# Kernel optimization log

Measured on AMD Instinct MI355X. Metric: run time of the kernel, lower is better.

The kernel has to match this reference:

```python
import math
import jax, jax.numpy as jnp
import numpy as np

B, T, DIN, D, L, K = 32, 4096, 256, 256, 2, 4
EPS = 1e-5
MIN_TS, MAX_TS = 10.0, 2000.0


def setup_inputs() -> dict:
    key = jax.random.key(0)
    ks = jax.random.split(key, 6)
    s = lambda k, shape: jax.random.normal(k, shape, jnp.float32) * 0.05
    return dict(
        x=jax.random.normal(ks[0], (B, T, DIN), jnp.float32),
        enc_w=s(ks[1], (D, DIN)),
        enc_b=jnp.zeros((D,), jnp.float32),
        enc_ln_g=jnp.ones((D,), jnp.float32),
        enc_ln_b=jnp.zeros((D,), jnp.float32),
        in_proj_w=s(ks[2], (L, 2 * D, D)),
        in_proj_b=jnp.zeros((L, 2 * D), jnp.float32),
        conv_w=s(ks[3], (L, D, K)),
        conv_b=jnp.zeros((L, D), jnp.float32),
        out_proj_w=s(ks[4], (L, D, D)),
        out_proj_b=jnp.zeros((L, D), jnp.float32),
        lnf_g=jnp.ones((D,), jnp.float32),
        lnf_b=jnp.zeros((D,), jnp.float32),
    )


def _ln(x, g, b):
    m = x.mean(-1, keepdims=True)
    v = ((x - m) ** 2).mean(-1, keepdims=True)
    return (x - m) * jax.lax.rsqrt(v + EPS) * g + b


def reference(x, enc_w, enc_b, enc_ln_g, enc_ln_b, in_proj_w, in_proj_b,
              conv_w, conv_b, out_proj_w, out_proj_b, lnf_g, lnf_b):
    # multi-timescale decay buffer (fixed, not learned)
    tau = jnp.exp(jnp.linspace(math.log(MIN_TS), math.log(MAX_TS), D))
    decay = jnp.exp(-1.0 / tau).astype(x.dtype)  # [D]

    def step(carry, x_t):
        h_states, bufs = carry  # [L,B,D], [L,B,D,K]
        # encoder: Linear -> LayerNorm -> ReLU
        h = jax.nn.relu(_ln(x_t @ enc_w.T + enc_b, enc_ln_g, enc_ln_b))
        new_h, new_buf = [], []
        for i in range(L):  # small fixed layer count
            xz = h @ in_proj_w[i].T + in_proj_b[i]          # [B,2D]
            x_in, z = xz[:, :D], xz[:, D:]
            # rolling depthwise-conv buffer: shift left, append x_in
            buf = jnp.concatenate([bufs[i][:, :, 1:], x_in[:, :, None]], axis=-1)  # [B,D,K]
            conv_out = jax.nn.silu(jnp.einsum('bdk,dk->bd', buf, conv_w[i]) + conv_b[i])
            hi = decay * h_states[i] + (1.0 - decay) * conv_out  # diagonal SSM update
            out = (hi * jax.nn.silu(z)) @ out_proj_w[i].T + out_proj_b[i]
            h = h + out  # residual
            new_h.append(hi)
            new_buf.append(buf)
        return (jnp.stack(new_h), jnp.stack(new_buf)), _ln(h, lnf_g, lnf_b)

    init = (jnp.zeros((L, B, D), x.dtype), jnp.zeros((L, B, D, K), x.dtype))
    _, ys = jax.lax.scan(step, init, jnp.swapaxes(x, 0, 1))  # ys: [T,B,D]
    return jnp.swapaxes(ys, 0, 1)  # [B,T,D]
```

## Files before the change

kernel.cpp:

```cpp
#include <hip/hip_runtime.h>
#include <hip/hip_bf16.h>
#include <math.h>

#define BB 32
#define TT 4096
#define DD 256
#define LL 2
#define NC 64
#define CH 64
#define MM (BB*TT)
#define EPSV 1e-5f

typedef __bf16 bf16;
typedef __attribute__((ext_vector_type(8))) __bf16 bf16x8;
typedef __attribute__((ext_vector_type(4))) __bf16 bf16x4;
typedef __attribute__((ext_vector_type(2))) __bf16 bf16x2;
typedef __attribute__((ext_vector_type(4))) float f32x4;

__device__ __forceinline__ float decay_of(int d) {
    const float l0 = 2.302585092994046f;
    const float l1 = 7.6009024595420815f;
    float lt = l0 + (float)d * (l1 - l0) * (1.0f / 255.0f);
    return expf(-expf(-lt));
}
__device__ __forceinline__ float silu_f(float v) { return v / (1.0f + expf(-v)); }

__global__ void cvtw_k(const float* __restrict__ we, const float* __restrict__ wi,
                       const float* __restrict__ wo, bf16* __restrict__ de,
                       bf16* __restrict__ di, bf16* __restrict__ dk)
{
    int i = blockIdx.x * 1024 + threadIdx.x;
    if (i < 65536)            de[i] = (bf16)we[i];
    else if (i < 327680)      di[i - 65536] = (bf16)wi[i - 65536];
    else if (i < 458752)      dk[i - 327680] = (bf16)wo[i - 327680];
}

template<int SRCF32, int EPI>
__global__ __launch_bounds__(256, 2)
void gemm_k(const void* __restrict__ Asrc,
            const bf16* __restrict__ W,
            const float* __restrict__ bias,
            const float* __restrict__ g1, const float* __restrict__ b1,
            bf16* __restrict__ O0, bf16* __restrict__ O1,
            float* __restrict__ Of)
{
    constexpr int NT = 16;
    constexpr int KCS = 8;
    constexpr int NSTAGE = 4;
    constexpr int KKS = 2;
    __shared__ bf16x8 ldsW[2048];

    const int tid = threadIdx.x;
    const int colblk = blockIdx.y * 256;
    const bf16* Wblk = W + (size_t)colblk * 256;

    const int wave = tid >> 6, lane = tid & 63;
    const int r = lane & 15, g4 = lane >> 4;
    const int c4 = g4 * 4;
    const size_t row = (size_t)blockIdx.x * 64 + wave * 16 + r;

    bf16x8 af[8];
    if (SRCF32) {
        const float* ap0 = (const float*)Asrc + row * 256;
        #pragma unroll
        for (int kk = 0; kk < 8; ++kk) {
            const float* ap = ap0 + kk * 32 + g4 * 8;
            float4 f0 = *(const float4*)ap;
            float4 f1 = *(const float4*)(ap + 4);
            bf16x8 t;
            t[0]=(bf16)f0.x; t[1]=(bf16)f0.y; t[2]=(bf16)f0.z; t[3]=(bf16)f0.w;
            t[4]=(bf16)f1.x; t[5]=(bf16)f1.y; t[6]=(bf16)f1.z; t[7]=(bf16)f1.w;
            af[kk] = t;
        }
    } else {
        const bf16* ap0 = (const bf16*)Asrc + row * 256;
        #pragma unroll
        for (int kk = 0; kk < 8; ++kk)
            af[kk] = *(const bf16x8*)(ap0 + kk * 32 + g4 * 8);
    }

    f32x4 acc[NT];
    #pragma unroll
    for (int nt = 0; nt < NT; ++nt) {
        float4 bv = *(const float4*)(bias + colblk + nt * 16 + c4);
        acc[nt] = (f32x4){bv.x, bv.y, bv.z, bv.w};
    }

    #pragma unroll
    for (int s = 0; s < NSTAGE; ++s) {
        if (s) __syncthreads();
        const int sBase = s * KCS;
        #pragma unroll
        for (int i = 0; i < 8; ++i) {
            int idx = tid + i * 256;
            int n   = idx >> 3;
            int kc  = idx & 7;
            int kcg = sBase + kc;
            ldsW[kc * 256 + (n ^ (kcg & 15))] =
                *(const bf16x8*)(Wblk + n * 256 + kcg * 8);
        }
        __syncthreads();
        #pragma unroll
        for (int kk = s * KKS; kk < (s + 1) * KKS; ++kk) {
            const int kcg = kk * 4 + g4;
            const int base = (kcg - sBase) * 256;
            const int swz = kcg & 15;
            #pragma unroll
            for (int nt = 0; nt < NT; ++nt) {
                bf16x8 bfr = ldsW[base + ((nt * 16 + r) ^ swz)];
                acc[nt] = __builtin_amdgcn_mfma_f32_16x16x32_bf16(bfr, af[kk], acc[nt], 0, 0, 0);
            }
        }
    }

    if (EPI == 1) {
        float s = 0.f, q = 0.f;
        #pragma unroll
        for (int nt = 0; nt < NT; ++nt)
            #pragma unroll
            for (int i = 0; i < 4; ++i) { float v = acc[nt][i]; s += v; q += v * v; }
        s += __shfl_xor(s, 16); q += __shfl_xor(q, 16);
        s += __shfl_xor(s, 32); q += __shfl_xor(q, 32);
        float mean = s * (1.0f / 256.0f);
        float rstd = rsqrtf(q * (1.0f / 256.0f) - mean * mean + EPSV);
        #pragma unroll
        for (int nt = 0; nt < NT; ++nt) {
            float4 gg = *(const float4*)(g1 + nt * 16 + c4);
            float4 bb = *(const float4*)(b1 + nt * 16 + c4);
            bf16x4 st;
            st[0] = (bf16)fmaxf((acc[nt][0] - mean) * rstd * gg.x + bb.x, 0.f);
            st[1] = (bf16)fmaxf((acc[nt][1] - mean) * rstd * gg.y + bb.y, 0.f);
            st[2] = (bf16)fmaxf((acc[nt][2] - mean) * rstd * gg.z + bb.z, 0.f);
            st[3] = (bf16)fmaxf((acc[nt][3] - mean) * rstd * gg.w + bb.w, 0.f);
            *(bf16x4*)(O0 + row * 256 + nt * 16 + c4) = st;
        }
    } else if (EPI == 2) {
        #pragma unroll
        for (int nt = 0; nt < NT; ++nt) {
            bf16* p = O0 + row * 256 + nt * 16 + c4;
            bf16x4 hv = *(const bf16x4*)p;
            bf16x4 st;
            #pragma unroll
            for (int i = 0; i < 4; ++i) st[i] = (bf16)(acc[nt][i] + (float)hv[i]);
            *(bf16x4*)p = st;
        }
    } else if (EPI == 3) {
        const int dosilu = (colblk >= 256);
        bf16* dst = dosilu ? O1 : O0;
        #pragma unroll
        for (int nt = 0; nt < NT; ++nt) {
            bf16x4 st;
            #pragma unroll
            for (int i = 0; i < 4; ++i) {
                float v = acc[nt][i];
                if (dosilu) v = silu_f(v);
                st[i] = (bf16)v;
            }
            *(bf16x4*)(dst + row * 256 + nt * 16 + c4) = st;
        }
    } else {
        #pragma unroll
        for (int nt = 0; nt < NT; ++nt) {
            bf16x4 hv = *(const bf16x4*)(O0 + row * 256 + nt * 16 + c4);
            #pragma unroll
            for (int i = 0; i < 4; ++i) acc[nt][i] += (float)hv[i];
        }
        float s = 0.f, q = 0.f;
        #pragma unroll
        for (int nt = 0; nt < NT; ++nt)
            #pragma unroll
            for (int i = 0; i < 4; ++i) { float v = acc[nt][i]; s += v; q += v * v; }
        s += __shfl_xor(s, 16); q += __shfl_xor(q, 16);
        s += __shfl_xor(s, 32); q += __shfl_xor(q, 32);
        float mean = s * (1.0f / 256.0f);
        float rstd = rsqrtf(q * (1.0f / 256.0f) - mean * mean + EPSV);
        #pragma unroll
        for (int nt = 0; nt < NT; ++nt) {
            float4 gg = *(const float4*)(g1 + nt * 16 + c4);
            float4 bb = *(const float4*)(b1 + nt * 16 + c4);
            float4 o;
            o.x = (acc[nt][0] - mean) * rstd * gg.x + bb.x;
            o.y = (acc[nt][1] - mean) * rstd * gg.y + bb.y;
            o.z = (acc[nt][2] - mean) * rstd * gg.z + bb.z;
            o.w = (acc[nt][3] - mean) * rstd * gg.w + bb.w;
            *(float4*)(Of + row * 256 + nt * 16 + c4) = o;
        }
    }
}

__global__ void pass1_k(const bf16* __restrict__ xc,
                        const float* __restrict__ cw, const float* __restrict__ cb,
                        float* __restrict__ cfin)
{
    const int d0 = threadIdx.x * 2;
    const int c = blockIdx.x, b = blockIdx.y;
    const int t0 = c * CH;
    const float w00=cw[d0*4+0], w01=cw[d0*4+1], w02=cw[d0*4+2], w03=cw[d0*4+3];
    const float w10=cw[d0*4+4], w11=cw[d0*4+5], w12=cw[d0*4+6], w13=cw[d0*4+7];
    const float bb0 = cb[d0], bb1 = cb[d0+1];
    const float a0 = decay_of(d0), a1 = decay_of(d0+1);
    const size_t base = (size_t)b * TT * 256 + d0;
    float x0m1=0,x0m2=0,x0m3=0, x1m1=0,x1m2=0,x1m3=0;
    if (t0 >= 1) { bf16x2 p = *(const bf16x2*)(xc + base + (size_t)(t0-1)*256); x0m1=(float)p[0]; x1m1=(float)p[1]; }
    if (t0 >= 2) { bf16x2 p = *(const bf16x2*)(xc + base + (size_t)(t0-2)*256); x0m2=(float)p[0]; x1m2=(float)p[1]; }
    if (t0 >= 3) { bf16x2 p = *(const bf16x2*)(xc + base + (size_t)(t0-3)*256); x0m3=(float)p[0]; x1m3=(float)p[1]; }
    float h0 = 0.f, h1 = 0.f;
    for (int t = t0; t < t0 + CH; ++t) {
        bf16x2 p = *(const bf16x2*)(xc + base + (size_t)t * 256);
        float xa = (float)p[0], xb = (float)p[1];
        float v0 = w03*xa + w02*x0m1 + w01*x0m2 + w00*x0m3 + bb0;
        float v1 = w13*xb + w12*x1m1 + w11*x1m2 + w10*x1m3 + bb1;
        h0 = a0*h0 + (1.f-a0)*silu_f(v0);
        h1 = a1*h1 + (1.f-a1)*silu_f(v1);
        x0m3=x0m2; x0m2=x0m1; x0m1=xa;
        x1m3=x1m2; x1m2=x1m1; x1m1=xb;
    }
    *(float2*)(cfin + ((size_t)b*NC + c)*256 + d0) = make_float2(h0, h1);
}

__global__ void scan2_k(const float* __restrict__ cfin, float* __restrict__ cin)
{
    const int d = threadIdx.x, b = blockIdx.x;
    float a = decay_of(d);
    float aC = a;
    #pragma unroll
    for (int j = 0; j < 6; ++j) aC *= aC;
    float H = 0.f;
    for (int c = 0; c < NC; ++c) {
        size_t o = ((size_t)b * NC + c) * 256 + d;
        cin[o] = H;
        H = aC * H + cfin[o];
    }
}

__global__ void pass3_k(const bf16* __restrict__ xc, const float* __restrict__ cin,
                        const float* __restrict__ cw, const float* __restrict__ cb,
                        bf16* __restrict__ szu)
{
    const int d0 = threadIdx.x * 2;
    const int c = blockIdx.x, b = blockIdx.y;
    const int t0 = c * CH;
    const float w00=cw[d0*4+0], w01=cw[d0*4+1], w02=cw[d0*4+2], w03=cw[d0*4+3];
    const float w10=cw[d0*4+4], w11=cw[d0*4+5], w12=cw[d0*4+6], w13=cw[d0*4+7];
    const float bb0 = cb[d0], bb1 = cb[d0+1];
    const float a0 = decay_of(d0), a1 = decay_of(d0+1);
    const size_t base = (size_t)b * TT * 256 + d0;
    float2 Hc = *(const float2*)(cin + ((size_t)b*NC + c)*256 + d0);
    float h0 = Hc.x, h1 = Hc.y;
    float x0m1=0,x0m2=0,x0m3=0, x1m1=0,x1m2=0,x1m3=0;
    if (t0 >= 1) { bf16x2 p = *(const bf16x2*)(xc + base + (size_t)(t0-1)*256); x0m1=(float)p[0]; x1m1=(float)p[1]; }
    if (t0 >= 2) { bf16x2 p = *(const bf16x2*)(xc + base + (size_t)(t0-2)*256); x0m2=(float)p[0]; x1m2=(float)p[1]; }
    if (t0 >= 3) { bf16x2 p = *(const bf16x2*)(xc + base + (size_t)(t0-3)*256); x0m3=(float)p[0]; x1m3=(float)p[1]; }
    for (int t = t0; t < t0 + CH; ++t) {
        bf16x2 p = *(const bf16x2*)(xc + base + (size_t)t * 256);
        float xa = (float)p[0], xb = (float)p[1];
        float v0 = w03*xa + w02*x0m1 + w01*x0m2 + w00*x0m3 + bb0;
        float v1 = w13*xb + w12*x1m1 + w11*x1m2 + w10*x1m3 + bb1;
        h0 = a0*h0 + (1.f-a0)*silu_f(v0);
        h1 = a1*h1 + (1.f-a1)*silu_f(v1);
        x0m3=x0m2; x0m2=x0m1; x0m1=xa;
        x1m3=x1m2; x1m2=x1m1; x1m1=xb;
        bf16* up = szu + base + (size_t)t * 256;
        bf16x2 sp = *(const bf16x2*)up;
        bf16x2 st;
        st[0] = (bf16)(h0 * (float)sp[0]);
        st[1] = (bf16)(h1 * (float)sp[1]);
        *(bf16x2*)up = st;
    }
}

extern "C" void kernel_launch(void* const* d_in, const int* in_sizes, int n_in,
                              void* d_out, int out_size, void* d_ws, size_t ws_size,
                              hipStream_t stream)
{
    (void)in_sizes; (void)n_in; (void)out_size;
    const float* x        = (const float*)d_in[0];
    const float* enc_w    = (const float*)d_in[1];
    const float* enc_b    = (const float*)d_in[2];
    const float* enc_ln_g = (const float*)d_in[3];
    const float* enc_ln_b = (const float*)d_in[4];
    const float* in_proj_w  = (const float*)d_in[5];
    const float* in_proj_b  = (const float*)d_in[6];
    const float* conv_w     = (const float*)d_in[7];
    const float* conv_b     = (const float*)d_in[8];
    const float* out_proj_w = (const float*)d_in[9];
    const float* out_proj_b = (const float*)d_in[10];
    const float* lnf_g      = (const float*)d_in[11];
    const float* lnf_b      = (const float*)d_in[12];

    if (ws_size < 139329536u) return;
    char* ws = (char*)d_ws;
    bf16*  h     = (bf16*)(ws);
    bf16*  szu   = (bf16*)(ws + 67108864);
    bf16*  wenc  = (bf16*)(ws + 134217728);
    bf16*  winp  = (bf16*)(ws + 134217728 + 131072);
    bf16*  woutp = (bf16*)(ws + 134217728 + 131072 + 524288);
    float* cfin  = (float*)(ws + 134217728 + 917504);
    float* cin   = (float*)(ws + 134217728 + 917504 + 2097152);
    bf16*  xc    = (bf16*)d_out;

    cvtw_k<<<dim3(448), dim3(1024), 0, stream>>>(enc_w, in_proj_w, out_proj_w,
                                                 wenc, winp, woutp);

    dim3 gblk(256);
    gemm_k<1, 1><<<dim3(2048, 1), gblk, 0, stream>>>(x, wenc, enc_b,
                                                    enc_ln_g, enc_ln_b, h, nullptr, nullptr);
    for (int l = 0; l < LL; ++l) {
        gemm_k<0, 3><<<dim3(2048, 2), gblk, 0, stream>>>(h, winp + (size_t)l * 512 * 256,
                                                        in_proj_b + l * 512, nullptr, nullptr,
                                                        xc, szu, nullptr);
        pass1_k<<<dim3(NC, BB), dim3(128), 0, stream>>>(xc, conv_w + l * DD * 4,
                                                        conv_b + l * DD, cfin);
        scan2_k<<<dim3(BB), dim3(256), 0, stream>>>(cfin, cin);
        pass3_k<<<dim3(NC, BB), dim3(128), 0, stream>>>(xc, cin, conv_w + l * DD * 4,
                                                        conv_b + l * DD, szu);
        if (l == 0) {
            gemm_k<0, 2><<<dim3(2048, 1), gblk, 0, stream>>>(szu, woutp,
                                                            out_proj_b, nullptr, nullptr,
                                                            h, nullptr, nullptr);
        } else {
            gemm_k<0, 4><<<dim3(2048, 1), gblk, 0, stream>>>(szu, woutp + (size_t)256 * 256,
                                                            out_proj_b + 256, lnf_g, lnf_b,
                                                            h, nullptr, (float*)d_out);
        }
    }
}
```

Baseline: 540.7 us.

## Use persistent narrow-column GEMM with resident weights for in/out projections

Adds a persistent GEMM kernel where each block owns a 64-column weight slice kept in LDS and loops over many row tiles, used for the in_proj and layer-0 out_proj GEMMs. This avoids reloading the full 256-column weight tile for every 64-row block and cuts the per-block synchronisation stages. The LayerNorm-epilogue GEMM is simplified to one column block with shared mean/variance code. In exchange, each row tile now needs only 4 accumulators, so A-fragments are reloaded once per column tile (8 or 4 times per row) and there is less MFMA work per A load.

```diff
diff --git a/kernel.cpp b/kernel.cpp
--- a/kernel.cpp
+++ b/kernel.cpp
@@ -35,14 +35,103 @@
     else if (i < 458752)      dk[i - 327680] = (bf16)wo[i - 327680];
 }
 
+template<int EPI, int NY, int BPS>
+__global__ __launch_bounds__(256, 2)
+void pgemm_k(const bf16* __restrict__ A,
+             const bf16* __restrict__ W,
+             const float* __restrict__ bias,
+             bf16* __restrict__ O0, bf16* __restrict__ O1)
+{
+    constexpr int TPB = 2048 / BPS;
+    __shared__ bf16x8 ldsW[2048];
+
+    const int tid = threadIdx.x;
+    const int ytile = (int)blockIdx.x % NY;
+    const int rowbase = (int)blockIdx.x / NY;
+    const int colblk = ytile * 64;
+    const bf16* Wblk = W + (size_t)colblk * 256;
+
+    #pragma unroll
+    for (int i = 0; i < 8; ++i) {
+        int idx = tid + i * 256;
+        int n  = idx >> 5;
+        int kc = idx & 31;
+        ldsW[kc * 64 + (n ^ (kc & 15))] = *(const bf16x8*)(Wblk + n * 256 + kc * 8);
+    }
+    __syncthreads();
+
+    const int wave = tid >> 6, lane = tid & 63;
+    const int r = lane & 15, g4 = lane >> 4;
+    const int c4 = g4 * 4;
+
+    float4 bv[4];
+    #pragma unroll
+    for (int nt = 0; nt < 4; ++nt)
+        bv[nt] = *(const float4*)(bias + colblk + nt * 16 + c4);
+
+    const int dosilu = (EPI == 3) && (colblk >= 256);
+    bf16* dst = (EPI == 3) ? (dosilu ? O1 : O0) : O0;
+    const int cb = (EPI == 3) ? (colblk & 255) : colblk;
+
+    #pragma unroll 1
+    for (int j = 0; j < TPB; ++j) {
+        const size_t row = (size_t)(rowbase + j * BPS) * 64 + wave * 16 + r;
+        const bf16* ap0 = A + row * 256;
+        bf16x8 af[8];
+        #pragma unroll
+        for (int kk = 0; kk < 8; ++kk)
+            af[kk] = *(const bf16x8*)(ap0 + kk * 32 + g4 * 8);
+
+        f32x4 acc[4];
+        #pragma unroll
+        for (int nt = 0; nt < 4; ++nt)
+            acc[nt] = (f32x4){bv[nt].x, bv[nt].y, bv[nt].z, bv[nt].w};
+
+        #pragma unroll
+        for (int kk = 0; kk < 8; ++kk) {
+            const int kc = kk * 4 + g4;
+            const int base = kc * 64;
+            const int swz = kc & 15;
+            #pragma unroll
+            for (int nt = 0; nt < 4; ++nt) {
+                bf16x8 bfr = ldsW[base + ((nt * 16 + r) ^ swz)];
+                acc[nt] = __builtin_amdgcn_mfma_f32_16x16x32_bf16(bfr, af[kk], acc[nt], 0, 0, 0);
+            }
+        }
+
+        if (EPI == 2) {
+            #pragma unroll
+            for (int nt = 0; nt < 4; ++nt) {
+                bf16* p = O0 + row * 256 + cb + nt * 16 + c4;
+                bf16x4 hv = *(const bf16x4*)p;
+                bf16x4 st;
+                #pragma unroll
+                for (int i = 0; i < 4; ++i) st[i] = (bf16)(acc[nt][i] + (float)hv[i]);
+                *(bf16x4*)p = st;
+            }
+        } else {
+            #pragma unroll
+            for (int nt = 0; nt < 4; ++nt) {
+                bf16x4 st;
+                #pragma unroll
+                for (int i = 0; i < 4; ++i) {
+                    float v = acc[nt][i];
+                    if (dosilu) v = silu_f(v);
+                    st[i] = (bf16)v;
+                }
+                *(bf16x4*)(dst + row * 256 + cb + nt * 16 + c4) = st;
+            }
+        }
+    }
+}
+
 template<int SRCF32, int EPI>
 __global__ __launch_bounds__(256, 2)
 void gemm_k(const void* __restrict__ Asrc,
             const bf16* __restrict__ W,
             const float* __restrict__ bias,
             const float* __restrict__ g1, const float* __restrict__ b1,
-            bf16* __restrict__ O0, bf16* __restrict__ O1,
-            float* __restrict__ Of)
+            bf16* __restrict__ O0, float* __restrict__ Of)
 {
     constexpr int NT = 16;
     constexpr int KCS = 8;
@@ -51,9 +140,6 @@
     __shared__ bf16x8 ldsW[2048];
 
     const int tid = threadIdx.x;
-    const int colblk = blockIdx.y * 256;
-    const bf16* Wblk = W + (size_t)colblk * 256;
-
     const int wave = tid >> 6, lane = tid & 63;
     const int r = lane & 15, g4 = lane >> 4;
     const int c4 = g4 * 4;
@@ -82,7 +168,7 @@
     f32x4 acc[NT];
     #pragma unroll
     for (int nt = 0; nt < NT; ++nt) {
-        float4 bv = *(const float4*)(bias + colblk + nt * 16 + c4);
+        float4 bv = *(const float4*)(bias + nt * 16 + c4);
         acc[nt] = (f32x4){bv.x, bv.y, bv.z, bv.w};
     }
 
@@ -97,7 +183,7 @@
             int kc  = idx & 7;
             int kcg = sBase + kc;
             ldsW[kc * 256 + (n ^ (kcg & 15))] =
-                *(const bf16x8*)(Wblk + n * 256 + kcg * 8);
+                *(const bf16x8*)(W + n * 256 + kcg * 8);
         }
         __syncthreads();
         #pragma unroll
@@ -113,16 +199,24 @@
         }
     }
 
+    if (EPI == 4) {
+        #pragma unroll
+        for (int nt = 0; nt < NT; ++nt) {
+            bf16x4 hv = *(const bf16x4*)(O0 + row * 256 + nt * 16 + c4);
+            #pragma unroll
+            for (int i = 0; i < 4; ++i) acc[nt][i] += (float)hv[i];
+        }
+    }
+    float s = 0.f, q = 0.f;
+    #pragma unroll
+    for (int nt = 0; nt < NT; ++nt)
+        #pragma unroll
+        for (int i = 0; i < 4; ++i) { float v = acc[nt][i]; s += v; q += v * v; }
+    s += __shfl_xor(s, 16); q += __shfl_xor(q, 16);
+    s += __shfl_xor(s, 32); q += __shfl_xor(q, 32);
+    float mean = s * (1.0f / 256.0f);
+    float rstd = rsqrtf(q * (1.0f / 256.0f) - mean * mean + EPSV);
     if (EPI == 1) {
-        float s = 0.f, q = 0.f;
-        #pragma unroll
-        for (int nt = 0; nt < NT; ++nt)
-            #pragma unroll
-            for (int i = 0; i < 4; ++i) { float v = acc[nt][i]; s += v; q += v * v; }
-        s += __shfl_xor(s, 16); q += __shfl_xor(q, 16);
-        s += __shfl_xor(s, 32); q += __shfl_xor(q, 32);
-        float mean = s * (1.0f / 256.0f);
-        float rstd = rsqrtf(q * (1.0f / 256.0f) - mean * mean + EPSV);
         #pragma unroll
         for (int nt = 0; nt < NT; ++nt) {
             float4 gg = *(const float4*)(g1 + nt * 16 + c4);
@@ -134,46 +228,7 @@
             st[3] = (bf16)fmaxf((acc[nt][3] - mean) * rstd * gg.w + bb.w, 0.f);
             *(bf16x4*)(O0 + row * 256 + nt * 16 + c4) = st;
         }
-    } else if (EPI == 2) {
-        #pragma unroll
-        for (int nt = 0; nt < NT; ++nt) {
-            bf16* p = O0 + row * 256 + nt * 16 + c4;
-            bf16x4 hv = *(const bf16x4*)p;
-            bf16x4 st;
-            #pragma unroll
-            for (int i = 0; i < 4; ++i) st[i] = (bf16)(acc[nt][i] + (float)hv[i]);
-            *(bf16x4*)p = st;
-        }
-    } else if (EPI == 3) {
-        const int dosilu = (colblk >= 256);
-        bf16* dst = dosilu ? O1 : O0;
-        #pragma unroll
-        for (int nt = 0; nt < NT; ++nt) {
-            bf16x4 st;
-            #pragma unroll
-            for (int i = 0; i < 4; ++i) {
-                float v = acc[nt][i];
-                if (dosilu) v = silu_f(v);
-                st[i] = (bf16)v;
-            }
-            *(bf16x4*)(dst + row * 256 + nt * 16 + c4) = st;
-        }
     } else {
-        #pragma unroll
-        for (int nt = 0; nt < NT; ++nt) {
-            bf16x4 hv = *(const bf16x4*)(O0 + row * 256 + nt * 16 + c4);
-            #pragma unroll
-            for (int i = 0; i < 4; ++i) acc[nt][i] += (float)hv[i];
-        }
-        float s = 0.f, q = 0.f;
-        #pragma unroll
-        for (int nt = 0; nt < NT; ++nt)
-            #pragma unroll
-            for (int i = 0; i < 4; ++i) { float v = acc[nt][i]; s += v; q += v * v; }
-        s += __shfl_xor(s, 16); q += __shfl_xor(q, 16);
-        s += __shfl_xor(s, 32); q += __shfl_xor(q, 32);
-        float mean = s * (1.0f / 256.0f);
-        float rstd = rsqrtf(q * (1.0f / 256.0f) - mean * mean + EPSV);
         #pragma unroll
         for (int nt = 0; nt < NT; ++nt) {
             float4 gg = *(const float4*)(g1 + nt * 16 + c4);
@@ -303,25 +358,23 @@
                                                  wenc, winp, woutp);
 
     dim3 gblk(256);
-    gemm_k<1, 1><<<dim3(2048, 1), gblk, 0, stream>>>(x, wenc, enc_b,
-                                                    enc_ln_g, enc_ln_b, h, nullptr, nullptr);
+    gemm_k<1, 1><<<dim3(2048), gblk, 0, stream>>>(x, wenc, enc_b,
+                                                  enc_ln_g, enc_ln_b, h, nullptr);
     for (int l = 0; l < LL; ++l) {
-        gemm_k<0, 3><<<dim3(2048, 2), gblk, 0, stream>>>(h, winp + (size_t)l * 512 * 256,
-                                                        in_proj_b + l * 512, nullptr, nullptr,
-                                                        xc, szu, nullptr);
+        pgemm_k<3, 8, 256><<<dim3(2048), gblk, 0, stream>>>(h, winp + (size_t)l * 512 * 256,
+                                                            in_proj_b + l * 512, xc, szu);
         pass1_k<<<dim3(NC, BB), dim3(128), 0, stream>>>(xc, conv_w + l * DD * 4,
                                                         conv_b + l * DD, cfin);
         scan2_k<<<dim3(BB), dim3(256), 0, stream>>>(cfin, cin);
         pass3_k<<<dim3(NC, BB), dim3(128), 0, stream>>>(xc, cin, conv_w + l * DD * 4,
                                                         conv_b + l * DD, szu);
         if (l == 0) {
-            gemm_k<0, 2><<<dim3(2048, 1), gblk, 0, stream>>>(szu, woutp,
-                                                            out_proj_b, nullptr, nullptr,
-                                                            h, nullptr, nullptr);
+            pgemm_k<2, 4, 512><<<dim3(2048), gblk, 0, stream>>>(szu, woutp,
+                                                                out_proj_b, h, nullptr);
         } else {
-            gemm_k<0, 4><<<dim3(2048, 1), gblk, 0, stream>>>(szu, woutp + (size_t)256 * 256,
-                                                            out_proj_b + 256, lnf_g, lnf_b,
-                                                            h, nullptr, (float*)d_out);
-        }
-    }
-}
+            gemm_k<0, 4><<<dim3(2048), gblk, 0, stream>>>(szu, woutp + (size_t)256 * 256,
+                                                          out_proj_b + 256, lnf_g, lnf_b,
+                                                          h, (float*)d_out);
+        }
+    }
+}
```

After: 603.5 us. +11.6%, slower.
